# Optimization experiments

Measured on AMD Instinct MI355X. Metric: run time of the kernel, lower is better.

Reference implementation:

```python
import jax, jax.numpy as jnp
import numpy as np

N = 100000        # nodes (== node_num)
E = 3200000       # edges
C = 8             # hidden (sparse=False branch)
HEADS = 2
GROUPS = 8
LAYERS = 3
FEAT = 16
EMB = 8
NCLS = 2


def glin(x, W, b):
    # PyG grouped Linear: x [..., C], W [G, C//G, C//G], b [C]
    G, cin, cout = W.shape
    xg = x.reshape(*x.shape[:-1], G, cin)
    out = jnp.einsum('...gi,gio->...go', xg, W)
    return out.reshape(*x.shape[:-1], G * cout) + b


def gcn_norm(edge_index, num_nodes):
    # symmetric GCN normalization with added self-loops, unit edge weights
    loop = jnp.arange(num_nodes, dtype=edge_index.dtype)
    src = jnp.concatenate([edge_index[0], loop])
    dst = jnp.concatenate([edge_index[1], loop])
    w = jnp.ones(src.shape[0], dtype=jnp.float32)
    deg = jax.ops.segment_sum(w, dst, num_segments=num_nodes)
    dinv = jnp.where(deg > 0, jax.lax.rsqrt(deg), 0.0)
    return src, dst, dinv[src] * dinv[dst]


def dna_conv(x_all, src, dst, norm, Wq, bq, Wk, bk, Wv, bv):
    # PyG DNAConv (eval mode): target's latest history entry attends over the
    # source neighbor's full history. x_all: [N, L, C].
    n, L, c = x_all.shape
    d = c // HEADS
    # q/k/v linears are per-entry -> compute per node, gather per edge (same math)
    q = glin(x_all[:, -1], Wq, bq).reshape(n, HEADS, d)    # [N,H,d]
    k = glin(x_all, Wk, bk).reshape(n, L, HEADS, d)        # [N,L,H,d]
    v = glin(x_all, Wv, bv).reshape(n, L, HEADS, d)
    qe = q[dst]                                            # [E',H,d]
    score = jnp.einsum('ehd,elhd->ehl', qe, k[src]) * (1.0 / np.sqrt(d))
    attn = jax.nn.softmax(score, axis=-1)                  # softmax over history L
    out = jnp.einsum('ehl,elhd->ehd', attn, v[src]).reshape(-1, c)
    out = out * norm[:, None]
    return jax.ops.segment_sum(out, dst, num_segments=n)   # aggr='add' at target


def setup_inputs():
    ks = jax.random.split(jax.random.key(0), 16)
    s = 0.5
    return {
        'x': jax.random.normal(ks[0], (N, FEAT), dtype=jnp.float32),
        'node_index': jnp.arange(N),
        'node_one_hot': jnp.zeros((N,), dtype=jnp.int32),
        'edge_index': jax.random.randint(ks[1], (2, E), 0, N),
        'edge_weight': jax.random.uniform(ks[2], (E,), dtype=jnp.float32),
        'emb_table': jax.random.normal(ks[3], (N, EMB), dtype=jnp.float32) * 0.1,
        'W1': jax.random.normal(ks[4], (EMB + FEAT, C), dtype=jnp.float32) * 0.2,
        'b1': jnp.zeros((C,), dtype=jnp.float32),
        'Wq': jax.random.normal(ks[5], (LAYERS, GROUPS, C // GROUPS, C // GROUPS), dtype=jnp.float32) * s,
        'bq': jnp.zeros((LAYERS, C), dtype=jnp.float32),
        'Wk': jax.random.normal(ks[6], (LAYERS, GROUPS, C // GROUPS, C // GROUPS), dtype=jnp.float32) * s,
        'bk': jnp.zeros((LAYERS, C), dtype=jnp.float32),
        'Wv': jax.random.normal(ks[7], (LAYERS, GROUPS, C // GROUPS, C // GROUPS), dtype=jnp.float32) * s,
        'bv': jnp.zeros((LAYERS, C), dtype=jnp.float32),
        'W2': jax.random.normal(ks[8], (C, NCLS), dtype=jnp.float32) * 0.3,
        'b2': jnp.zeros((NCLS,), dtype=jnp.float32),
    }


def reference(x, node_index, node_one_hot, edge_index, edge_weight,
              emb_table, W1, b1, Wq, bq, Wk, bk, Wv, bv, W2, b2):
    # node_one_hot / edge_weight are unpacked but unused in the original forward
    h = jnp.concatenate([emb_table[node_index], x], axis=1)   # [N, EMB+FEAT]
    h = jax.nn.relu(h @ W1 + b1)                              # [N, C]
    x_all = h[:, None, :]                                     # history [N, 1, C]
    src, dst, norm = gcn_norm(edge_index, x.shape[0])
    for i in range(LAYERS):
        h = jax.nn.relu(dna_conv(x_all, src, dst, norm,
                                 Wq[i], bq[i], Wk[i], bk[i], Wv[i], bv[i]))
        x_all = jnp.concatenate([x_all, h[:, None, :]], axis=1)
    logits = x_all[:, -1] @ W2 + b2
    return jax.nn.log_softmax(logits, axis=-1)
```

## Files before the change

kernel.cpp:

```cpp
#include <hip/hip_runtime.h>
#include <math.h>


#define SBB   8
#define SBN   256
#define CH    8192
#define CAP   9216

typedef _Float16 half8 __attribute__((ext_vector_type(8)));

__global__ void __launch_bounds__(256) phaseAC(const int* __restrict__ eidx,
                                               int* __restrict__ gcnt,
                                               int* __restrict__ ebuf,
                                               int E, int NS) {
    __shared__ int sorted_[CH];
    __shared__ unsigned short karr[CH];
    __shared__ int cntS[512];
    __shared__ int lofs[512];
    __shared__ int wbase[512];
    __shared__ int sA[512], sB[512];
    int t = threadIdx.x, b = blockIdx.x;
    int base = b * CH;
    int nEdge = E - base; if (nEdge > CH) nEdge = CH;

    for (int i = t; i < 512; i += 256) cntS[i] = 0;
    __syncthreads();

    int w[32]; short kk[32];
#pragma unroll
    for (int it = 0; it < 8; it++) {
        int e0 = base + (it * 256 + t) * 4;
        if (e0 + 3 < E) {
            int4 s4 = *(const int4*)(eidx + e0);
            int4 d4 = *(const int4*)(eidx + E + e0);
            int ss[4] = { s4.x, s4.y, s4.z, s4.w };
            int dd[4] = { d4.x, d4.y, d4.z, d4.w };
#pragma unroll
            for (int j = 0; j < 4; j++) {
                int idx = it * 4 + j;
                w[idx] = ss[j] | ((dd[j] & (SBN - 1)) << 17);
                kk[idx] = (short)(dd[j] >> SBB);
                atomicAdd(&cntS[kk[idx]], 1);
            }
        } else {
#pragma unroll
            for (int j = 0; j < 4; j++) {
                int e = e0 + j, idx = it * 4 + j;
                if (e < E) {
                    int s = eidx[e], d = eidx[E + e];
                    w[idx] = s | ((d & (SBN - 1)) << 17);
                    kk[idx] = (short)(d >> SBB);
                    atomicAdd(&cntS[kk[idx]], 1);
                } else { w[idx] = 0; kk[idx] = 511; }
            }
        }
    }
    __syncthreads();
    sA[t] = cntS[t]; sA[t + 256] = cntS[t + 256];
    __syncthreads();
    int* sp = sA; int* dp = sB;
    for (int o = 1; o < 512; o <<= 1) {
#pragma unroll
        for (int h = 0; h < 2; h++) {
            int i = t + h * 256;
            int v = sp[i];
            if (i >= o) v += sp[i - o];
            dp[i] = v;
        }
        __syncthreads();
        int* tmp = sp; sp = dp; dp = tmp;
    }
    for (int i = t; i < 512; i += 256) {
        int excl = sp[i] - cntS[i];
        lofs[i] = excl;
        if (i < NS && cntS[i] > 0) {
            int g = atomicAdd(&gcnt[i], cntS[i]);
            wbase[i] = i * CAP + g - excl;
        }
    }
    __syncthreads();
#pragma unroll
    for (int idx = 0; idx < 32; idx++) {
        if (kk[idx] != 511) {
            int p = atomicAdd(&lofs[kk[idx]], 1);
            sorted_[p] = w[idx];
            karr[p] = (unsigned short)kk[idx];
        }
    }
    __syncthreads();
    for (int i = t; i < nEdge; i += 256)
        ebuf[wbase[karr[i]] + i] = sorted_[i];
}

__global__ void super_csr(int* __restrict__ ebuf, const int* __restrict__ gcnt,
                          unsigned int* __restrict__ off, char* __restrict__ A,
                          char* __restrict__ U, int NS, int n) {
    __shared__ int seg[CAP];
    __shared__ int cnt[SBN];
    __shared__ int fillp[SBN];
    __shared__ int sd[256];
    int t = threadIdx.x, k = blockIdx.x;
    cnt[t] = 0;
    int start = k * CAP;
    int len = gcnt[k];
    __syncthreads();
    for (int i = t; i < len; i += 256) {
        int w = ebuf[start + i];
        seg[i] = w;
        atomicAdd(&cnt[w >> 17], 1);
    }
    __syncthreads();
    int v = cnt[t];
    sd[t] = v; __syncthreads();
    for (int o = 1; o < 256; o <<= 1) {
        int u = 0; if (t >= o) u = sd[t - o];
        __syncthreads(); sd[t] += u; __syncthreads();
    }
    int excl = sd[t] - v;
    fillp[t] = excl;
    int d = (k << SBB) + t;
    if (d < n) {
        off[d] = (unsigned int)(start + excl) | ((unsigned int)v << 22);
        float dv = rsqrtf((float)(v + 1));
        *(float*)(A + (size_t)d * 32 + 16) = dv;
        *(float*)(U + (size_t)d * 64 + 48) = dv;
    }
    __syncthreads();
    for (int i = t; i < len; i += 256) {
        int w = seg[i];
        int pos = atomicAdd(&fillp[w >> 17], 1);
        ebuf[start + pos] = w & 131071;
    }
}

__global__ void node_init(const float* __restrict__ x, const int* __restrict__ nidx,
                          const float* __restrict__ emb, const float* __restrict__ W1,
                          const float* __restrict__ b1, char* __restrict__ A,
                          char* __restrict__ U, int n) {
    int i = blockIdx.x * blockDim.x + threadIdx.x;
    if (i >= n) return;
    float in[24];
    int ni = nidx[i];
    const float4* ep = (const float4*)(emb + (size_t)ni * 8);
    float4 e0 = ep[0], e1 = ep[1];
    in[0] = e0.x; in[1] = e0.y; in[2] = e0.z; in[3] = e0.w;
    in[4] = e1.x; in[5] = e1.y; in[6] = e1.z; in[7] = e1.w;
    const float4* xp = (const float4*)(x + (size_t)i * 16);
#pragma unroll
    for (int t = 0; t < 4; t++) {
        float4 v = xp[t];
        in[8 + 4 * t + 0] = v.x; in[8 + 4 * t + 1] = v.y;
        in[8 + 4 * t + 2] = v.z; in[8 + 4 * t + 3] = v.w;
    }
    float acc[8];
#pragma unroll
    for (int j = 0; j < 8; j++) acc[j] = b1[j];
#pragma unroll
    for (int t = 0; t < 24; t++) {
        float xv = in[t];
#pragma unroll
        for (int j = 0; j < 8; j++) acc[j] = fmaf(xv, W1[t * 8 + j], acc[j]);
    }
    half8 h;
#pragma unroll
    for (int j = 0; j < 8; j++) h[j] = (_Float16)fmaxf(acc[j], 0.0f);
    *(half8*)(A + (size_t)i * 32) = h;
    *(half8*)(U + (size_t)i * 64) = h;
}

template <int Li>
__device__ __forceinline__ void attn_out(const float* xs, const float* qv,
                                         const float* __restrict__ wk, const float* __restrict__ bk,
                                         const float* __restrict__ wv, const float* __restrict__ bv,
                                         float* out) {
    float score[2][Li];
#pragma unroll
    for (int l = 0; l < Li; l++) {
#pragma unroll
        for (int h = 0; h < 2; h++) {
            float sc = 0.f;
#pragma unroll
            for (int dd = 0; dd < 4; dd++) {
                int c = h * 4 + dd;
                sc = fmaf(qv[c], fmaf(xs[l * 8 + c], wk[c], bk[c]), sc);
            }
            score[h][l] = 0.5f * sc;
        }
    }
    float attn[2][Li];
#pragma unroll
    for (int h = 0; h < 2; h++) {
        float m = score[h][0];
#pragma unroll
        for (int l = 1; l < Li; l++) m = fmaxf(m, score[h][l]);
        float ssum = 0.f;
#pragma unroll
        for (int l = 0; l < Li; l++) { attn[h][l] = __expf(score[h][l] - m); ssum += attn[h][l]; }
        float inv = 1.0f / ssum;
#pragma unroll
        for (int l = 0; l < Li; l++) attn[h][l] *= inv;
    }
#pragma unroll
    for (int c = 0; c < 8; c++) {
        int h = c >> 2;
        float o = 0.f;
#pragma unroll
        for (int l = 0; l < Li; l++) o = fmaf(attn[h][l], fmaf(xs[l * 8 + c], wv[c], bv[c]), o);
        out[c] = o;
    }
}

template <int Li, bool LAST>
__global__ void agg_layer(const int* __restrict__ ssrc, const unsigned int* __restrict__ off,
                          const char* __restrict__ A, char* __restrict__ U,
                          const float* __restrict__ wq, const float* __restrict__ bq,
                          const float* __restrict__ wk, const float* __restrict__ bk,
                          const float* __restrict__ wv, const float* __restrict__ bv,
                          const float* __restrict__ W2, const float* __restrict__ b2,
                          float* __restrict__ out, int n) {
    int tid = blockIdx.x * blockDim.x + threadIdx.x;
    int d = tid >> 3, t = tid & 7;
    if (d >= n) return;
    unsigned int ow = off[d];
    int lo = (int)(ow & 0x3FFFFFu), cnt = (int)(ow >> 22);

    float qv[8];
    {
        half8 qh;
        if (Li == 1) qh = *(const half8*)(A + (size_t)d * 32);
        else         qh = *(const half8*)(U + (size_t)d * 64 + (Li - 1) * 16);
#pragma unroll
        for (int c = 0; c < 8; c++) qv[c] = fmaf((float)qh[c], wq[c], bq[c]);
    }

    float acc[8];
#pragma unroll
    for (int c = 0; c < 8; c++) acc[c] = 0.f;

    for (int j = t; j < cnt + 1; j += 8) {
        int s = (j == 0) ? d : ssrc[lo + j - 1];
        float xs[8 * Li];
        float ns;
        if (Li == 1) {
            half8 h = *(const half8*)(A + (size_t)s * 32);
#pragma unroll
            for (int c = 0; c < 8; c++) xs[c] = (float)h[c];
            ns = *(const float*)(A + (size_t)s * 32 + 16);
        } else {
            const char* ub = U + (size_t)s * 64;
#pragma unroll
            for (int l = 0; l < Li; l++) {
                half8 h = *(const half8*)(ub + l * 16);
#pragma unroll
                for (int c = 0; c < 8; c++) xs[l * 8 + c] = (float)h[c];
            }
            ns = *(const float*)(ub + 48);
        }
        float o[8];
        attn_out<Li>(xs, qv, wk, bk, wv, bv, o);
#pragma unroll
        for (int c = 0; c < 8; c++) acc[c] = fmaf(o[c], ns, acc[c]);
    }
#pragma unroll
    for (int m = 1; m < 8; m <<= 1) {
#pragma unroll
        for (int c = 0; c < 8; c++) acc[c] += __shfl_xor(acc[c], m);
    }
    float nd = (Li == 1) ? *(const float*)(A + (size_t)d * 32 + 16)
                         : *(const float*)(U + (size_t)d * 64 + 48);
    if (!LAST) {
        float h = fmaxf(acc[t] * nd, 0.f);
        *(_Float16*)(U + (size_t)d * 64 + Li * 16 + 2 * t) = (_Float16)h;
    } else if (t == 0) {
        float z0 = b2[0], z1 = b2[1];
#pragma unroll
        for (int c = 0; c < 8; c++) {
            float h = fmaxf(acc[c] * nd, 0.f);
            z0 = fmaf(h, W2[c * 2 + 0], z0);
            z1 = fmaf(h, W2[c * 2 + 1], z1);
        }
        float m = fmaxf(z0, z1);
        float lse = m + logf(__expf(z0 - m) + __expf(z1 - m));
        ((float2*)out)[d] = make_float2(z0 - lse, z1 - lse);
    }
}

extern "C" void kernel_launch(void* const* d_in, const int* in_sizes, int n_in,
                              void* d_out, int out_size, void* d_ws, size_t ws_size,
                              hipStream_t stream) {
    const float* x    = (const float*)d_in[0];
    const int*   nidx = (const int*)d_in[1];
    const int*   eidx = (const int*)d_in[3];
    const float* emb  = (const float*)d_in[5];
    const float* W1   = (const float*)d_in[6];
    const float* b1   = (const float*)d_in[7];
    const float* Wq   = (const float*)d_in[8];
    const float* bq   = (const float*)d_in[9];
    const float* Wk   = (const float*)d_in[10];
    const float* bk   = (const float*)d_in[11];
    const float* Wv   = (const float*)d_in[12];
    const float* bv   = (const float*)d_in[13];
    const float* W2   = (const float*)d_in[14];
    const float* b2   = (const float*)d_in[15];
    float* out = (float*)d_out;

    const int n = in_sizes[0] / 16;
    const int E = in_sizes[3] / 2;
    const int NS = (n + SBN - 1) / SBN;
    const int NBLK = (E + CH - 1) / CH;

    char* wsp = (char*)d_ws;
    char*  A     = wsp;                 wsp += (size_t)n * 32;
    char*  U     = wsp;                 wsp += (size_t)n * 64;
    int*   ebuf  = (int*)wsp;           wsp += (size_t)NS * CAP * 4;
    unsigned int* off = (unsigned int*)wsp;  wsp += (size_t)n * 4;
    int*   gcnt  = (int*)wsp;           wsp += (size_t)NS * 4;

    dim3 blk(256);
    dim3 gn((n + 255) / 256);
    dim3 ga(((size_t)n * 8 + 255) / 256);

    hipMemsetAsync(gcnt, 0, (size_t)NS * 4, stream);
    phaseAC<<<NBLK, blk, 0, stream>>>(eidx, gcnt, ebuf, E, NS);
    super_csr<<<NS, blk, 0, stream>>>(ebuf, gcnt, off, A, U, NS, n);
    node_init<<<gn, blk, 0, stream>>>(x, nidx, emb, W1, b1, A, U, n);

    agg_layer<1, false><<<ga, blk, 0, stream>>>(ebuf, off, A, U,
        Wq, bq, Wk, bk, Wv, bv, W2, b2, out, n);
    agg_layer<2, false><<<ga, blk, 0, stream>>>(ebuf, off, A, U,
        Wq + 8, bq + 8, Wk + 8, bk + 8, Wv + 8, bv + 8, W2, b2, out, n);
    agg_layer<3, true><<<ga, blk, 0, stream>>>(ebuf, off, A, U,
        Wq + 16, bq + 16, Wk + 16, bk + 16, Wv + 16, bv + 16, W2, b2, out, n);
}
```

Baseline: 278.4 us.

## Halve bucketing chunk, add nontemporal loads, batch neighbor gathers in aggregation

The edge bucketing kernel now processes 4096 edges per block instead of 8192, which lowers per-thread register arrays and launches more blocks. Edge loads in bucketing and the CSR build use nontemporal hints. The aggregation kernel gives each of the 8 lanes a contiguous slice of neighbors rather than a strided one, and issues four neighbor gathers before computing so more loads are in flight. The risks are higher register pressure in the unrolled gather and less coalesced reads of the ssrc indices, since each lane now walks its own slice.

```diff
diff --git a/kernel.cpp b/kernel.cpp
--- a/kernel.cpp
+++ b/kernel.cpp
@@ -4,10 +4,11 @@
 
 #define SBB   8
 #define SBN   256
-#define CH    8192
+#define CH    4096
 #define CAP   9216
 
 typedef _Float16 half8 __attribute__((ext_vector_type(8)));
+typedef int int4v __attribute__((ext_vector_type(4)));
 
 __global__ void __launch_bounds__(256) phaseAC(const int* __restrict__ eidx,
                                                int* __restrict__ gcnt,
@@ -26,20 +27,18 @@
     for (int i = t; i < 512; i += 256) cntS[i] = 0;
     __syncthreads();
 
-    int w[32]; short kk[32];
-#pragma unroll
-    for (int it = 0; it < 8; it++) {
+    int w[16]; short kk[16];
+#pragma unroll
+    for (int it = 0; it < 4; it++) {
         int e0 = base + (it * 256 + t) * 4;
         if (e0 + 3 < E) {
-            int4 s4 = *(const int4*)(eidx + e0);
-            int4 d4 = *(const int4*)(eidx + E + e0);
-            int ss[4] = { s4.x, s4.y, s4.z, s4.w };
-            int dd[4] = { d4.x, d4.y, d4.z, d4.w };
+            int4v s4 = __builtin_nontemporal_load((const int4v*)(eidx + e0));
+            int4v d4 = __builtin_nontemporal_load((const int4v*)(eidx + E + e0));
 #pragma unroll
             for (int j = 0; j < 4; j++) {
                 int idx = it * 4 + j;
-                w[idx] = ss[j] | ((dd[j] & (SBN - 1)) << 17);
-                kk[idx] = (short)(dd[j] >> SBB);
+                w[idx] = s4[j] | ((d4[j] & (SBN - 1)) << 17);
+                kk[idx] = (short)(d4[j] >> SBB);
                 atomicAdd(&cntS[kk[idx]], 1);
             }
         } else {
@@ -80,7 +79,7 @@
     }
     __syncthreads();
 #pragma unroll
-    for (int idx = 0; idx < 32; idx++) {
+    for (int idx = 0; idx < 16; idx++) {
         if (kk[idx] != 511) {
             int p = atomicAdd(&lofs[kk[idx]], 1);
             sorted_[p] = w[idx];
@@ -105,7 +104,7 @@
     int len = gcnt[k];
     __syncthreads();
     for (int i = t; i < len; i += 256) {
-        int w = ebuf[start + i];
+        int w = __builtin_nontemporal_load(&ebuf[start + i]);
         seg[i] = w;
         atomicAdd(&cnt[w >> 17], 1);
     }
@@ -121,9 +120,9 @@
     int d = (k << SBB) + t;
     if (d < n) {
         off[d] = (unsigned int)(start + excl) | ((unsigned int)v << 22);
-        float dv = rsqrtf((float)(v + 1));
-        *(float*)(A + (size_t)d * 32 + 16) = dv;
-        *(float*)(U + (size_t)d * 64 + 48) = dv;
+        float dvv = rsqrtf((float)(v + 1));
+        *(float*)(A + (size_t)d * 32 + 16) = dvv;
+        *(float*)(U + (size_t)d * 64 + 48) = dvv;
     }
     __syncthreads();
     for (int i = t; i < len; i += 256) {
@@ -224,47 +223,66 @@
     unsigned int ow = off[d];
     int lo = (int)(ow & 0x3FFFFFu), cnt = (int)(ow >> 22);
 
+    half8 qh;
+    if (Li == 1) qh = *(const half8*)(A + (size_t)d * 32);
+    else if (Li == 2) qh = *(const half8*)(U + (size_t)d * 64 + 16);
+    else qh = *(const half8*)(U + (size_t)d * 64 + 32);
     float qv[8];
-    {
-        half8 qh;
-        if (Li == 1) qh = *(const half8*)(A + (size_t)d * 32);
-        else         qh = *(const half8*)(U + (size_t)d * 64 + (Li - 1) * 16);
-#pragma unroll
-        for (int c = 0; c < 8; c++) qv[c] = fmaf((float)qh[c], wq[c], bq[c]);
-    }
+#pragma unroll
+    for (int c = 0; c < 8; c++) qv[c] = fmaf((float)qh[c], wq[c], bq[c]);
 
     float acc[8];
 #pragma unroll
     for (int c = 0; c < 8; c++) acc[c] = 0.f;
 
-    for (int j = t; j < cnt + 1; j += 8) {
-        int s = (j == 0) ? d : ssrc[lo + j - 1];
-        float xs[8 * Li];
-        float ns;
-        if (Li == 1) {
-            half8 h = *(const half8*)(A + (size_t)s * 32);
-#pragma unroll
-            for (int c = 0; c < 8; c++) xs[c] = (float)h[c];
-            ns = *(const float*)(A + (size_t)s * 32 + 16);
-        } else {
-            const char* ub = U + (size_t)s * 64;
-#pragma unroll
-            for (int l = 0; l < Li; l++) {
-                half8 h = *(const half8*)(ub + l * 16);
-#pragma unroll
-                for (int c = 0; c < 8; c++) xs[l * 8 + c] = (float)h[c];
-            }
-            ns = *(const float*)(ub + 48);
-        }
-        float o[8];
-        attn_out<Li>(xs, qv, wk, bk, wv, bv, o);
-#pragma unroll
-        for (int c = 0; c < 8; c++) acc[c] = fmaf(o[c], ns, acc[c]);
-    }
-#pragma unroll
-    for (int m = 1; m < 8; m <<= 1) {
-#pragma unroll
-        for (int c = 0; c < 8; c++) acc[c] += __shfl_xor(acc[c], m);
+    int total = cnt + 1;
+    int g = (total + 7) >> 3;
+    int j0 = t * g;
+    int j1 = j0 + g; if (j1 > total) j1 = total;
+
+    for (int j = j0; j < j1; j += 4) {
+        int m = j1 - j; if (m > 4) m = 4;
+        int sidx[4];
+#pragma unroll
+        for (int u = 0; u < 4; u++) {
+            int idx = j + u;
+            sidx[u] = (u < m) ? ((idx == 0) ? d : ssrc[lo + idx - 1]) : d;
+        }
+        half8 r[4][Li]; float nsv[4];
+#pragma unroll
+        for (int u = 0; u < 4; u++) {
+            if (u < m) {
+                if (Li == 1) {
+                    const char* p = A + (size_t)sidx[u] * 32;
+                    r[u][0] = *(const half8*)p;
+                    nsv[u] = *(const float*)(p + 16);
+                } else {
+                    const char* p = U + (size_t)sidx[u] * 64;
+#pragma unroll
+                    for (int l = 0; l < Li; l++) r[u][l] = *(const half8*)(p + l * 16);
+                    nsv[u] = *(const float*)(p + 48);
+                }
+            }
+        }
+#pragma unroll
+        for (int u = 0; u < 4; u++) {
+            if (u < m) {
+                float xs[8 * Li];
+#pragma unroll
+                for (int l = 0; l < Li; l++)
+#pragma unroll
+                    for (int c = 0; c < 8; c++) xs[l * 8 + c] = (float)r[u][l][c];
+                float o[8];
+                attn_out<Li>(xs, qv, wk, bk, wv, bv, o);
+#pragma unroll
+                for (int c = 0; c < 8; c++) acc[c] = fmaf(o[c], nsv[u], acc[c]);
+            }
+        }
+    }
+#pragma unroll
+    for (int m2 = 1; m2 < 8; m2 <<= 1) {
+#pragma unroll
+        for (int c = 0; c < 8; c++) acc[c] += __shfl_xor(acc[c], m2);
     }
     float nd = (Li == 1) ? *(const float*)(A + (size_t)d * 32 + 16)
                          : *(const float*)(U + (size_t)d * 64 + 48);
@@ -279,8 +297,8 @@
             z0 = fmaf(h, W2[c * 2 + 0], z0);
             z1 = fmaf(h, W2[c * 2 + 1], z1);
         }
-        float m = fmaxf(z0, z1);
-        float lse = m + logf(__expf(z0 - m) + __expf(z1 - m));
+        float m2 = fmaxf(z0, z1);
+        float lse = m2 + logf(__expf(z0 - m2) + __expf(z1 - m2));
         ((float2*)out)[d] = make_float2(z0 - lse, z1 - lse);
     }
 }
@@ -310,17 +328,17 @@
     const int NBLK = (E + CH - 1) / CH;
 
     char* wsp = (char*)d_ws;
-    char*  A     = wsp;                 wsp += (size_t)n * 32;
-    char*  U     = wsp;                 wsp += (size_t)n * 64;
-    int*   ebuf  = (int*)wsp;           wsp += (size_t)NS * CAP * 4;
+    char*  A     = wsp;                      wsp += (size_t)n * 32;
+    char*  U     = wsp;                      wsp += (size_t)n * 64;
+    int*   ebuf  = (int*)wsp;                wsp += (size_t)NS * CAP * 4;
     unsigned int* off = (unsigned int*)wsp;  wsp += (size_t)n * 4;
-    int*   gcnt  = (int*)wsp;           wsp += (size_t)NS * 4;
+    int*   gcnt  = (int*)wsp;                wsp += (size_t)NS * 4;
 
     dim3 blk(256);
     dim3 gn((n + 255) / 256);
     dim3 ga(((size_t)n * 8 + 255) / 256);
 
-    hipMemsetAsync(gcnt, 0, (size_t)NS * 4, stream);
+    (void)hipMemsetAsync(gcnt, 0, (size_t)NS * 4, stream);
     phaseAC<<<NBLK, blk, 0, stream>>>(eidx, gcnt, ebuf, E, NS);
     super_csr<<<NS, blk, 0, stream>>>(ebuf, gcnt, off, A, U, NS, n);
     node_init<<<gn, blk, 0, stream>>>(x, nidx, emb, W1, b1, A, U, n);
```

Measured after the change: 276.8 us. No clear change (-0.6%).
